# Kernel tuning notes

Hardware: AMD Instinct MI355X
Metric: run time of the kernel (lower is better)

## Reference

```python
import jax, jax.numpy as jnp
import numpy as np

M = 8192        # tokens (batch*seq)
K = 14336       # d_ff (input features of down proj)
N = 4096        # d_model (output features)
GROUP = 128     # quantization group size along K


def unpack_int4(w_packed):
    """[N, K//8] int32 -> [N, K] signed int4 values in [-8, 7] (float32)."""
    n, kp = w_packed.shape
    shifts = (jnp.arange(8, dtype=jnp.int32) * 4)  # nibble 0 = lowest bits
    nib = (w_packed[:, :, None] >> shifts) & 0xF   # [N, K//8, 8]
    nib = nib - jnp.where(nib >= 8, 16, 0)         # sign-extend 4-bit
    return nib.reshape(n, kp * 8).astype(jnp.float32)


def setup_inputs() -> dict:
    key = jax.random.key(0)
    ks = jax.random.split(key, 6)
    qx = jax.random.normal(ks[0], (M, K), dtype=jnp.float32)
    qxscale = jax.random.uniform(ks[1], (M, 1), dtype=jnp.float32) * 0.05 + 0.001
    residual = jax.random.normal(ks[2], (M, N), dtype=jnp.float32)
    weight_i4 = jax.random.randint(ks[3], (N, K // 8), jnp.iinfo(jnp.int32).min,
                                   jnp.iinfo(jnp.int32).max, dtype=jnp.int32)
    weight_scale = jax.random.uniform(ks[4], (N, K // GROUP), dtype=jnp.float32) * 0.02 + 0.001
    bias = jax.random.normal(ks[5], (N,), dtype=jnp.float32)
    return {"qx": qx, "qxscale": qxscale, "residual": residual,
            "weight_i4": weight_i4, "weight_scale": weight_scale,
            "bias": bias, "group_size": GROUP}


def reference(qx, qxscale, residual, weight_i4, weight_scale, bias, group_size):
    # 1) unpack int32 -> signed int4
    iw = unpack_int4(weight_i4)                          # [N, K]
    n, k = iw.shape
    g = k // group_size
    # 2) group-wise dequantize (one scale per group along K, per output row)
    dq = (iw.reshape(n, g, group_size) * weight_scale[:, :, None]).reshape(n, k)
    # 3) matmul x @ W^T, 4) per-token scale, residual + bias
    y = jnp.einsum('mk,nk->mn', qx, dq) * qxscale + residual + bias
    return y
```

## Files before the change

### kernel.cpp

```cpp
#include <hip/hip_runtime.h>
#include <hip/hip_bf16.h>
#include <stdint.h>

#define M_DIM 8192
#define K_DIM 14336
#define N_DIM 4096
#define GROUP_SZ 128
#define NGROUP (K_DIM / GROUP_SZ)

typedef short short8 __attribute__((ext_vector_type(8)));
typedef float f32x4 __attribute__((ext_vector_type(4)));
typedef int i32x4 __attribute__((ext_vector_type(4)));

static __device__ __forceinline__ short f2bf(float f) {
  unsigned u = __builtin_bit_cast(unsigned, f);
  u += 0x7FFFu + ((u >> 16) & 1u);
  return (short)(u >> 16);
}

static __device__ __forceinline__ void gload_lds16(const void* g, void* lds) {
  __builtin_amdgcn_global_load_lds(
      (const __attribute__((address_space(1))) unsigned int*)g,
      (__attribute__((address_space(3))) unsigned int*)lds, 16, 0, 0);
}


__global__ __launch_bounds__(256) void dp_quant_x(const float* __restrict__ x,
                                                  char* __restrict__ xq,
                                                  float* __restrict__ sx) {
  __shared__ float rowbuf[K_DIM];
  __shared__ float red[256];
  const int row = blockIdx.x;
  const int t = threadIdx.x;
  const float* xr = x + (size_t)row * K_DIM;
  float amax = 0.f;
#pragma unroll
  for (int j = 0; j < 14; ++j) {
    float4 v = *(const float4*)(xr + j * 1024 + t * 4);
    *(float4*)(rowbuf + j * 1024 + t * 4) = v;
    amax = fmaxf(amax,
                 fmaxf(fmaxf(fabsf(v.x), fabsf(v.y)), fmaxf(fabsf(v.z), fabsf(v.w))));
  }
  red[t] = amax;
  __syncthreads();
  for (int s = 128; s > 0; s >>= 1) {
    if (t < s) red[t] = fmaxf(red[t], red[t + s]);
    __syncthreads();
  }
  const float am = red[0];
  const float inv = (am > 0.f) ? 127.f / am : 0.f;
  if (t == 0) sx[row] = am * (1.f / 127.f);
  char* xo = xq + (size_t)row * K_DIM;
#pragma unroll
  for (int j = 0; j < 14; ++j) {
    float4 v = *(const float4*)(rowbuf + j * 1024 + t * 4);
    char4 q;
    q.x = (char)__float2int_rn(v.x * inv);
    q.y = (char)__float2int_rn(v.y * inv);
    q.z = (char)__float2int_rn(v.z * inv);
    q.w = (char)__float2int_rn(v.w * inv);
    *(char4*)(xo + j * 1024 + t * 4) = q;
  }
}

__global__ __launch_bounds__(256) void dp_repack_w(const int* __restrict__ wq,
                                                   const float* __restrict__ wsc,
                                                   char* __restrict__ w8,
                                                   float* __restrict__ sw) {
  __shared__ float wsl[NGROUP];
  const int n = blockIdx.x;
  const int t = threadIdx.x;
  if (t < NGROUP) wsl[t] = wsc[(size_t)n * NGROUP + t];
  __syncthreads();
  float mx = 0.f;
#pragma unroll
  for (int g = 0; g < NGROUP; ++g) mx = fmaxf(mx, wsl[g]);
  const float invsw = 15.875f / mx;
  if (t == 0) sw[n] = mx * (8.f / 127.f);
#pragma unroll
  for (int j = 0; j < 7; ++j) {
    int p = t + 256 * j;
    int w = wq[(size_t)n * (K_DIM / 8) + p];
    float sc = wsl[p >> 4] * invsw;
    unsigned lo = 0, hi = 0;
#pragma unroll
    for (int b = 0; b < 4; ++b) {
      int q = (w << (28 - 4 * b)) >> 28;
      int r = __float2int_rn((float)q * sc);
      lo |= (unsigned)(r & 0xff) << (8 * b);
    }
#pragma unroll
    for (int b = 4; b < 8; ++b) {
      int q = (w << (28 - 4 * b)) >> 28;
      int r = __float2int_rn((float)q * sc);
      hi |= (unsigned)(r & 0xff) << (8 * (b - 4));
    }
    *(uint2*)(w8 + (size_t)n * K_DIM + (size_t)p * 8) = make_uint2(lo, hi);
  }
}

__global__ __launch_bounds__(512, 2) void dp_gemm8i(
    const char* __restrict__ Xq, const char* __restrict__ Wq8,
    const float* __restrict__ sw, const float* __restrict__ sx,
    const float* __restrict__ qxscale, const float* __restrict__ residual,
    const float* __restrict__ bias, float* __restrict__ out) {
  __shared__ __align__(16) char lds[131072];

  const int tid = threadIdx.x;
  const int lane = tid & 63;
  const int wid = tid >> 6;
  const int wm = wid >> 2, wn = wid & 3;
  const int lr = lane & 15, lg = lane >> 4;

  const int wg = blockIdx.x;
  const int swz = (wg & 7) * 64 + (wg >> 3);
  const int m0 = (swz >> 4) * 256;
  const int n0 = (swz & 15) * 256;

  int offA[4][2], offB[2][2];
#pragma unroll
  for (int mf = 0; mf < 4; ++mf) {
    int r = wm * 64 + mf * 16 + lr;
#pragma unroll
    for (int kk = 0; kk < 2; ++kk)
      offA[mf][kk] = r * 128 + (((kk * 4 + lg) ^ (r & 7)) << 4);
  }
#pragma unroll
  for (int nf = 0; nf < 2; ++nf) {
    int r = wn * 32 + nf * 16 + lr;
#pragma unroll
    for (int kk = 0; kk < 2; ++kk)
      offB[nf][kk] = r * 128 + (((kk * 4 + lg) ^ (r & 7)) << 4);
  }

  const int srow = tid >> 3;
  const int ksrc = ((tid & 7) ^ (srow & 7)) * 16;
  const size_t aRow = (size_t)(m0 + srow) * K_DIM + ksrc;
  const size_t bRow = (size_t)(n0 + srow) * K_DIM + ksrc;
  const int dst0 = tid * 16;

  i32x4 acc[8][4];
#pragma unroll
  for (int i = 0; i < 8; ++i)
#pragma unroll
    for (int j = 0; j < 4; ++j) acc[i][j] = (i32x4){0, 0, 0, 0};

  i32x4 aF[4][2];
  i32x4 bF[2][2][2];

#define STAGE_A(T, h)                                                          \
  do {                                                                         \
    size_t g_ = aRow + (size_t)((h) * 128) * K_DIM + (size_t)(T) * 128;        \
    int d_ = (((T) & 1) << 15) + ((h) << 14) + dst0;                           \
    gload_lds16(Xq + g_, lds + d_);                                            \
    gload_lds16(Xq + g_ + (size_t)64 * K_DIM, lds + d_ + 8192);                \
  } while (0)

#define STAGE_B(T, h)                                                          \
  do {                                                                         \
    size_t g_ = bRow + (size_t)((h) * 128) * K_DIM + (size_t)(T) * 128;        \
    int d_ = 65536 + (((T) & 1) << 15) + ((h) << 14) + dst0;                   \
    gload_lds16(Wq8 + g_, lds + d_);                                           \
    gload_lds16(Wq8 + g_ + (size_t)64 * K_DIM, lds + d_ + 8192);               \
  } while (0)

#define FENCE asm volatile("" ::: "memory")

#define INTERVAL(T, mh, LB, STMT, WMT)                                         \
  do {                                                                         \
    if (LB) {                                                                  \
      _Pragma("unroll") for (int nh = 0; nh < 2; ++nh) {                       \
        const char* Bb_ = lds + (65536 + (((T) & 1) << 15) + (nh << 14));      \
        _Pragma("unroll") for (int nf = 0; nf < 2; ++nf)                       \
            _Pragma("unroll") for (int kk = 0; kk < 2; ++kk)                   \
                bF[nh][nf][kk] = *(const i32x4*)(Bb_ + offB[nf][kk]);          \
      }                                                                        \
    }                                                                          \
    {                                                                          \
      const char* Ab_ = lds + ((((T) & 1) << 15) + ((mh) << 14));              \
      _Pragma("unroll") for (int mf = 0; mf < 4; ++mf)                         \
          _Pragma("unroll") for (int kk = 0; kk < 2; ++kk)                     \
              aF[mf][kk] = *(const i32x4*)(Ab_ + offA[mf][kk]);                \
    }                                                                          \
    STMT;                                                                      \
    FENCE;                                                                     \
    WMT;                                                                       \
    __builtin_amdgcn_s_barrier();                                              \
    FENCE;                                                                     \
    __builtin_amdgcn_s_setprio(1);                                             \
    _Pragma("unroll") for (int nh = 0; nh < 2; ++nh)                           \
        _Pragma("unroll") for (int kk = 0; kk < 2; ++kk)                       \
            _Pragma("unroll") for (int mf = 0; mf < 4; ++mf)                   \
                _Pragma("unroll") for (int nf = 0; nf < 2; ++nf)               \
                    acc[(mh) * 4 + mf][nh * 2 + nf] =                          \
                        __builtin_amdgcn_mfma_i32_16x16x64_i8(                 \
                            aF[mf][kk], bF[nh][nf][kk],                        \
                            acc[(mh) * 4 + mf][nh * 2 + nf], 0, 0, 0);         \
    __builtin_amdgcn_s_setprio(0);                                             \
    FENCE;                                                                     \
  } while (0)

  STAGE_A(0, 0); STAGE_B(0, 0); STAGE_A(0, 1); STAGE_B(0, 1);
  STAGE_A(1, 0); STAGE_B(1, 0);
  FENCE;
  asm volatile("s_waitcnt vmcnt(4)" ::: "memory");
  __builtin_amdgcn_s_barrier();
  FENCE;

  for (int i = 0; i < 56; ++i) {
    const int t = 2 * i;
    const bool st = (i < 55);
    INTERVAL(t, 0, 1, { STAGE_A(t + 1, 1); STAGE_B(t + 1, 1); }, {});
    INTERVAL(t, 1, 0, { if (st) { STAGE_A(t + 2, 0); STAGE_B(t + 2, 0); } },
             {
               if (st) asm volatile("s_waitcnt vmcnt(4)" ::: "memory");
               else    asm volatile("s_waitcnt vmcnt(0)" ::: "memory");
             });
    INTERVAL(t + 1, 0, 1, { if (st) { STAGE_A(t + 2, 1); STAGE_B(t + 2, 1); } }, {});
    INTERVAL(t + 1, 1, 0, { if (st) { STAGE_A(t + 3, 0); STAGE_B(t + 3, 0); } },
             {
               if (st) asm volatile("s_waitcnt vmcnt(4)" ::: "memory");
               else    asm volatile("s_waitcnt vmcnt(0)" ::: "memory");
             });
  }

#pragma unroll
  for (int mh = 0; mh < 2; ++mh)
#pragma unroll
    for (int mf = 0; mf < 4; ++mf)
#pragma unroll
      for (int nh = 0; nh < 2; ++nh)
#pragma unroll
        for (int nf = 0; nf < 2; ++nf) {
          int n = n0 + nh * 128 + wn * 32 + nf * 16 + lr;
          float bv = bias[n];
          float swn = sw[n];
          i32x4 v = acc[mh * 4 + mf][nh * 2 + nf];
#pragma unroll
          for (int rr = 0; rr < 4; ++rr) {
            int m = m0 + mh * 128 + wm * 64 + mf * 16 + lg * 4 + rr;
            size_t off = (size_t)m * N_DIM + n;
            out[off] = (float)v[rr] * (qxscale[m] * sx[m] * swn) + residual[off] + bv;
          }
        }
#undef INTERVAL
#undef STAGE_A
#undef STAGE_B
#undef FENCE
}


__global__ __launch_bounds__(256) void dp_dequant_w(const int* __restrict__ wq,
                                                    const float* __restrict__ wsc,
                                                    short* __restrict__ wb) {
  int p = blockIdx.x * 256 + threadIdx.x;
  int n = blockIdx.y;
  int w = wq[(size_t)n * (K_DIM / 8) + p];
  float sc = wsc[(size_t)n * NGROUP + (p >> 4)];
  short8 v;
#pragma unroll
  for (int j = 0; j < 8; ++j) {
    int q = (w << (28 - 4 * j)) >> 28;
    v[j] = f2bf((float)q * sc);
  }
  *(short8*)(wb + (size_t)n * K_DIM + (size_t)p * 8) = v;
}

template <int BMODE>
__global__ __launch_bounds__(256) void dp_gemm(
    const float* __restrict__ qx, const int* __restrict__ Wq,
    const float* __restrict__ Wsc, const short* __restrict__ Wb,
    const float* __restrict__ qxscale, const float* __restrict__ residual,
    const float* __restrict__ bias, float* __restrict__ out) {
  __shared__ short As[128 * 64];
  __shared__ short Bs[128 * 64];

  const int tid = threadIdx.x;
  const int lane = tid & 63;
  const int w = tid >> 6;

  const int nwg = gridDim.x;
  const int cpx = nwg >> 3;
  const int wg = blockIdx.x;
  const int swz = (wg & 7) * cpx + (wg >> 3);
  const int bm = swz / (N_DIM / 128);
  const int bn = swz % (N_DIM / 128);
  const int m0 = bm * 128, n0 = bn * 128;

  const int wm = w >> 1, wn = w & 1;
  const int lr = lane & 15, lg = lane >> 4;

  f32x4 acc[4][4];
#pragma unroll
  for (int i = 0; i < 4; ++i)
#pragma unroll
    for (int j = 0; j < 4; ++j) acc[i][j] = (f32x4){0.f, 0.f, 0.f, 0.f};

  for (int kt = 0; kt < K_DIM / 64; ++kt) {
    const int k0 = kt * 64;
#pragma unroll
    for (int i = 0; i < 4; ++i) {
      int ldsb = i * 4096 + tid * 16;
      int row = ldsb >> 7;
      int slog = ((ldsb >> 4) & 7) ^ (row & 7);
      const float4* p = (const float4*)(qx + (size_t)(m0 + row) * K_DIM + k0 + slog * 8);
      float4 u0 = p[0], u1 = p[1];
      short8 v;
      v[0] = f2bf(u0.x); v[1] = f2bf(u0.y); v[2] = f2bf(u0.z); v[3] = f2bf(u0.w);
      v[4] = f2bf(u1.x); v[5] = f2bf(u1.y); v[6] = f2bf(u1.z); v[7] = f2bf(u1.w);
      *(short8*)((char*)As + ldsb) = v;
    }
    if (BMODE == 0) {
#pragma unroll
      for (int i = 0; i < 4; ++i) {
        int ldsb = i * 4096 + w * 1024 + lane * 16;
        int row = ldsb >> 7;
        int slog = ((ldsb >> 4) & 7) ^ (row & 7);
        gload_lds16(Wb + (size_t)(n0 + row) * K_DIM + k0 + slog * 8, (char*)Bs + ldsb);
      }
    } else {
      int row = tid >> 1;
      int kb = (tid & 1) * 32;
      int4 pw = *(const int4*)(Wq + (size_t)(n0 + row) * (K_DIM / 8) + (k0 + kb) / 8);
      float sc = Wsc[(size_t)(n0 + row) * NGROUP + (k0 + kb) / GROUP_SZ];
      int pv[4] = {pw.x, pw.y, pw.z, pw.w};
#pragma unroll
      for (int p = 0; p < 4; ++p) {
        short8 v;
#pragma unroll
        for (int j = 0; j < 8; ++j) {
          int q = (pv[p] << (28 - 4 * j)) >> 28;
          v[j] = f2bf((float)q * sc);
        }
        int slog = (tid & 1) * 4 + p;
        int sp = slog ^ (row & 7);
        *(short8*)((char*)Bs + row * 128 + sp * 16) = v;
      }
    }
    __syncthreads();
#pragma unroll
    for (int s = 0; s < 2; ++s) {
      short8 a[4], b[4];
#pragma unroll
      for (int f = 0; f < 4; ++f) {
        int row = wm * 64 + f * 16 + lr;
        int sp = (s * 4 + lg) ^ (row & 7);
        a[f] = *(const short8*)((char*)As + row * 128 + sp * 16);
      }
#pragma unroll
      for (int f = 0; f < 4; ++f) {
        int row = wn * 64 + f * 16 + lr;
        int sp = (s * 4 + lg) ^ (row & 7);
        b[f] = *(const short8*)((char*)Bs + row * 128 + sp * 16);
      }
#pragma unroll
      for (int i = 0; i < 4; ++i)
#pragma unroll
        for (int j = 0; j < 4; ++j)
          acc[i][j] = __builtin_amdgcn_mfma_f32_16x16x32_bf16(a[i], b[j], acc[i][j], 0, 0, 0);
    }
    __syncthreads();
  }

  const int mb = m0 + wm * 64, nb = n0 + wn * 64;
#pragma unroll
  for (int i = 0; i < 4; ++i)
#pragma unroll
    for (int j = 0; j < 4; ++j) {
      int n = nb + j * 16 + lr;
      float bv = bias[n];
#pragma unroll
      for (int r = 0; r < 4; ++r) {
        int m = mb + i * 16 + lg * 4 + r;
        size_t off = (size_t)m * N_DIM + n;
        out[off] = acc[i][j][r] * qxscale[m] + residual[off] + bv;
      }
    }
}

extern "C" void kernel_launch(void* const* d_in, const int* in_sizes, int n_in,
                              void* d_out, int out_size, void* d_ws, size_t ws_size,
                              hipStream_t stream) {
  const float* qx = (const float*)d_in[0];
  const float* qxscale = (const float*)d_in[1];
  const float* residual = (const float*)d_in[2];
  const int* wq = (const int*)d_in[3];
  const float* wsc = (const float*)d_in[4];
  const float* bias = (const float*)d_in[5];
  float* out = (float*)d_out;

  const size_t SZ_W8 = (size_t)N_DIM * K_DIM;
  const size_t SZ_XQ = (size_t)M_DIM * K_DIM;
  const size_t OFF_XQ = SZ_W8;
  const size_t OFF_SW = OFF_XQ + SZ_XQ;
  const size_t OFF_SX = OFF_SW + (size_t)N_DIM * 4;
  const size_t need_i8 = OFF_SX + (size_t)M_DIM * 4;
  const size_t need_w = (size_t)N_DIM * K_DIM * 2;

  if (ws_size >= need_i8) {
    char* w8 = (char*)d_ws;
    char* xq = (char*)d_ws + OFF_XQ;
    float* sw = (float*)((char*)d_ws + OFF_SW);
    float* sx = (float*)((char*)d_ws + OFF_SX);
    dp_repack_w<<<dim3(N_DIM), dim3(256), 0, stream>>>(wq, wsc, w8, sw);
    dp_quant_x<<<dim3(M_DIM), dim3(256), 0, stream>>>(qx, xq, sx);
    dp_gemm8i<<<dim3((M_DIM / 256) * (N_DIM / 256)), dim3(512), 0, stream>>>(
        xq, w8, sw, sx, qxscale, residual, bias, out);
  } else if (ws_size >= need_w) {
    short* wb = (short*)d_ws;
    dp_dequant_w<<<dim3(K_DIM / 8 / 256, N_DIM), dim3(256), 0, stream>>>(wq, wsc, wb);
    dp_gemm<0><<<dim3(2048), dim3(256), 0, stream>>>(qx, wq, wsc, wb, qxscale,
                                                     residual, bias, out);
  } else {
    dp_gemm<1><<<dim3(2048), dim3(256), 0, stream>>>(qx, wq, wsc, nullptr, qxscale,
                                                     residual, bias, out);
  }
}
```

Baseline: 511.0 us.

## Load int8 weight fragments directly from global memory instead of staging through LDS

```diff
diff --git a/kernel.cpp b/kernel.cpp
--- a/kernel.cpp
+++ b/kernel.cpp
@@ -104,7 +104,7 @@
     const float* __restrict__ sw, const float* __restrict__ sx,
     const float* __restrict__ qxscale, const float* __restrict__ residual,
     const float* __restrict__ bias, float* __restrict__ out) {
-  __shared__ __align__(16) char lds[131072];
+  __shared__ __align__(16) char lds[65536];
 
   const int tid = threadIdx.x;
   const int lane = tid & 63;
@@ -117,27 +117,21 @@
   const int m0 = (swz >> 4) * 256;
   const int n0 = (swz & 15) * 256;
 
-  int offA[4][2], offB[2][2];
+  int offA[4][2];
 #pragma unroll
   for (int mf = 0; mf < 4; ++mf) {
     int r = wm * 64 + mf * 16 + lr;
 #pragma unroll
     for (int kk = 0; kk < 2; ++kk)
       offA[mf][kk] = r * 128 + (((kk * 4 + lg) ^ (r & 7)) << 4);
-  }
-#pragma unroll
-  for (int nf = 0; nf < 2; ++nf) {
-    int r = wn * 32 + nf * 16 + lr;
-#pragma unroll
-    for (int kk = 0; kk < 2; ++kk)
-      offB[nf][kk] = r * 128 + (((kk * 4 + lg) ^ (r & 7)) << 4);
   }
 
   const int srow = tid >> 3;
   const int ksrc = ((tid & 7) ^ (srow & 7)) * 16;
   const size_t aRow = (size_t)(m0 + srow) * K_DIM + ksrc;
-  const size_t bRow = (size_t)(n0 + srow) * K_DIM + ksrc;
   const int dst0 = tid * 16;
+
+  const char* bPtr = Wq8 + (size_t)(n0 + wn * 32 + lr) * K_DIM + lg * 16;
 
   i32x4 acc[8][4];
 #pragma unroll
@@ -156,26 +150,22 @@
     gload_lds16(Xq + g_ + (size_t)64 * K_DIM, lds + d_ + 8192);                \
   } while (0)
 
-#define STAGE_B(T, h)                                                          \
+#define LOAD_B(Tb)                                                             \
   do {                                                                         \
-    size_t g_ = bRow + (size_t)((h) * 128) * K_DIM + (size_t)(T) * 128;        \
-    int d_ = 65536 + (((T) & 1) << 15) + ((h) << 14) + dst0;                   \
-    gload_lds16(Wq8 + g_, lds + d_);                                           \
-    gload_lds16(Wq8 + g_ + (size_t)64 * K_DIM, lds + d_ + 8192);               \
-  } while (0)
-
-#define FENCE asm volatile("" ::: "memory")
-
-#define INTERVAL(T, mh, LB, STMT, WMT)                                         \
-  do {                                                                         \
-    if (LB) {                                                                  \
-      _Pragma("unroll") for (int nh = 0; nh < 2; ++nh) {                       \
-        const char* Bb_ = lds + (65536 + (((T) & 1) << 15) + (nh << 14));      \
+    const char* bp_ = bPtr + (size_t)(Tb) * 128;                               \
+    _Pragma("unroll") for (int nh = 0; nh < 2; ++nh)                           \
         _Pragma("unroll") for (int nf = 0; nf < 2; ++nf)                       \
             _Pragma("unroll") for (int kk = 0; kk < 2; ++kk)                   \
-                bF[nh][nf][kk] = *(const i32x4*)(Bb_ + offB[nf][kk]);          \
-      }                                                                        \
-    }                                                                          \
+                bF[nh][nf][kk] = *(const i32x4*)(                              \
+                    bp_ + (size_t)(nh * 128 + nf * 16) * K_DIM + kk * 64);     \
+  } while (0)
+
+#define FENCE asm volatile("" ::: "memory")
+
+#define INTERVAL(T, mh, LDB, STMT, WMT)                                        \
+  do {                                                                         \
+    if (LDB) { LOAD_B(T); }                                                    \
+    FENCE;                                                                     \
     {                                                                          \
       const char* Ab_ = lds + ((((T) & 1) << 15) + ((mh) << 14));              \
       _Pragma("unroll") for (int mf = 0; mf < 4; ++mf)                         \
@@ -200,26 +190,25 @@
     FENCE;                                                                     \
   } while (0)
 
-  STAGE_A(0, 0); STAGE_B(0, 0); STAGE_A(0, 1); STAGE_B(0, 1);
-  STAGE_A(1, 0); STAGE_B(1, 0);
+  STAGE_A(0, 0); STAGE_A(0, 1); STAGE_A(1, 0);
   FENCE;
-  asm volatile("s_waitcnt vmcnt(4)" ::: "memory");
+  asm volatile("s_waitcnt vmcnt(2)" ::: "memory");
   __builtin_amdgcn_s_barrier();
   FENCE;
 
   for (int i = 0; i < 56; ++i) {
     const int t = 2 * i;
     const bool st = (i < 55);
-    INTERVAL(t, 0, 1, { STAGE_A(t + 1, 1); STAGE_B(t + 1, 1); }, {});
-    INTERVAL(t, 1, 0, { if (st) { STAGE_A(t + 2, 0); STAGE_B(t + 2, 0); } },
+    INTERVAL(t, 0, 1, { STAGE_A(t + 1, 1); }, {});
+    INTERVAL(t, 1, 0, { if (st) STAGE_A(t + 2, 0); },
              {
-               if (st) asm volatile("s_waitcnt vmcnt(4)" ::: "memory");
+               if (st) asm volatile("s_waitcnt vmcnt(2)" ::: "memory");
                else    asm volatile("s_waitcnt vmcnt(0)" ::: "memory");
              });
-    INTERVAL(t + 1, 0, 1, { if (st) { STAGE_A(t + 2, 1); STAGE_B(t + 2, 1); } }, {});
-    INTERVAL(t + 1, 1, 0, { if (st) { STAGE_A(t + 3, 0); STAGE_B(t + 3, 0); } },
+    INTERVAL(t + 1, 0, 1, { if (st) STAGE_A(t + 2, 1); }, {});
+    INTERVAL(t + 1, 1, 0, { if (st) STAGE_A(t + 3, 0); },
              {
-               if (st) asm volatile("s_waitcnt vmcnt(4)" ::: "memory");
+               if (st) asm volatile("s_waitcnt vmcnt(2)" ::: "memory");
                else    asm volatile("s_waitcnt vmcnt(0)" ::: "memory");
              });
   }
@@ -244,8 +233,8 @@
           }
         }
 #undef INTERVAL
+#undef LOAD_B
 #undef STAGE_A
-#undef STAGE_B
 #undef FENCE
 }
 
```

Measured after the change: 815.9 us. +59.7%, slower.
